# Optimization experiments

Hardware: AMD Instinct MI355X
Metric: run time of the kernel (lower is better)

The kernel has to match this reference:

```python
import jax, jax.numpy as jnp
import numpy as np
from jax import lax

PALETTE = 256


def setup_inputs() -> dict:
    key = jax.random.key(0)
    k1, k2, k3, k4 = jax.random.split(key, 4)
    x = jax.random.normal(k1, (16, 64, 256, 256), dtype=jnp.float32)
    lookup_table = jax.random.normal(k2, (PALETTE,), dtype=jnp.float32) * 0.05
    weight_idx = jax.random.randint(k3, (64, 64, 3, 3), 0, PALETTE, dtype=jnp.int32)
    bias = jax.random.normal(k4, (64,), dtype=jnp.float32) * 0.01
    return {"x": x, "lookup_table": lookup_table, "weight_idx": weight_idx, "bias": bias}


def reference(x, lookup_table, weight_idx, bias):
    # Dequantize: palette gather produces full OIHW weight tensor.
    full_w = lookup_table[weight_idx]  # [O, I, kH, kW] float32
    # conv2d with stride=1, padding=0 (hardcoded in module), dilation=1, groups=1
    out = lax.conv_general_dilated(
        x, full_w,
        window_strides=(1, 1),
        padding='VALID',
        rhs_dilation=(1, 1),
        dimension_numbers=('NCHW', 'OIHW', 'NCHW'),
        feature_group_count=1,
    )
    return out + bias[None, :, None, None]
```

## Files before the change

kernel.cpp:

```cpp
#include <hip/hip_runtime.h>


typedef __bf16 bf16x8 __attribute__((ext_vector_type(8)));
typedef float f32x4 __attribute__((ext_vector_type(4)));

union Frag {
    uint4 q;
    bf16x8 v;
};

__global__ __launch_bounds__(256) void dequant_B(
        const float* __restrict__ lut, const int* __restrict__ widx,
        uint4* __restrict__ Bws) {
    int s = blockIdx.x * 256 + threadIdx.x;
    int l = s & 63;
    int nt = (s >> 6) & 3;
    int kc = s >> 8;
    if (kc >= 18) return;
    int r = kc >> 1;
    int kh = r / 3, kw = r - kh * 3;
    int o = nt * 16 + (l & 15);
    int c0 = (kc & 1) * 32 + (l >> 4) * 8;
    Frag f;
#pragma unroll
    for (int j = 0; j < 8; ++j) {
        int c = c0 + j;
        int idx = widx[((o * 64 + c) * 3 + kh) * 3 + kw];
        f.v[j] = (__bf16)lut[idx];
    }
    Bws[s] = f.q;
}

#define LDS_PIX 396

__global__ __launch_bounds__(256, 3) void conv_mfma(
        const float* __restrict__ x, const float* __restrict__ bias,
        const uint4* __restrict__ Bws, float* __restrict__ out) {
    __shared__ uint4 ldsA[8 * LDS_PIX];
    unsigned* lds32 = (unsigned*)ldsA;

    int bx = blockIdx.x;
    int ow0 = (bx & 3) * 64;
    int oh0 = ((bx >> 2) & 63) * 4;
    int n = bx >> 8;
    int t = threadIdx.x;

    const float* xn = x + (size_t)n * (64 * 256 * 256);

    int w = t >> 6;
    int l = t & 63;
    int l15 = l & 15, l4 = l >> 4;

    {
        int colg = l15;
        int chp  = l4;
        const float* xw = xn + ow0 + colg * 4;
#pragma unroll
        for (int cc = 0; cc < 2; ++cc) {
            int cb = w + cc * 4;
            const float* cbase = xw + (cb * 8 + chp * 2) * 65536;
            f32x4 f0[6], f1[6];
#pragma unroll
            for (int rr = 0; rr < 6; ++rr) {
                int y = oh0 + rr; if (y > 255) y = 255;
                const float* p = cbase + y * 256;
                f0[rr] = *(const f32x4*)(p);
                f1[rr] = *(const f32x4*)(p + 65536);
            }
#pragma unroll
            for (int rr = 0; rr < 6; ++rr) {
                int gbase = cb * LDS_PIX + rr * 66 + colg * 4;
#pragma unroll
                for (int i = 0; i < 4; ++i) {
                    union { __bf16 h[2]; unsigned u; } bp;
                    bp.h[0] = (__bf16)f0[rr][i];
                    bp.h[1] = (__bf16)f1[rr][i];
                    lds32[(gbase + i) * 4 + chp] = bp.u;
                }
            }
        }
        if (t < 96) {
            int cblk = t & 7;
            int rc = t >> 3;
            int rr = rc >> 1;
            int col2 = 64 + (rc & 1);
            int y = oh0 + rr; if (y > 255) y = 255;
            int xc = ow0 + col2; if (xc > 255) xc = 255;
            const float* src = xn + cblk * 8 * 65536 + y * 256 + xc;
            Frag f;
#pragma unroll
            for (int j = 0; j < 8; ++j)
                f.v[j] = (__bf16)src[j * 65536];
            ldsA[cblk * LDS_PIX + rr * 66 + col2] = f.q;
        }
    }
    __syncthreads();

    f32x4 acc[4][4] = {};

    for (int kc = 0; kc < 18; ++kc) {
        int r = kc >> 1;
        int kh = r / 3, kw = r - kh * 3;
        int cblk = (kc & 1) * 4 + l4;
        int pix = (w + kh) * 66 + l15 + kw;

        Frag b[4];
#pragma unroll
        for (int nt = 0; nt < 4; ++nt)
            b[nt].q = Bws[(kc * 4 + nt) * 64 + l];

        Frag a[4];
#pragma unroll
        for (int mt = 0; mt < 4; ++mt)
            a[mt].q = ldsA[cblk * LDS_PIX + pix + mt * 16];

#pragma unroll
        for (int mt = 0; mt < 4; ++mt)
#pragma unroll
            for (int nt = 0; nt < 4; ++nt)
                acc[mt][nt] = __builtin_amdgcn_mfma_f32_16x16x32_bf16(
                    a[mt].v, b[nt].v, acc[mt][nt], 0, 0, 0);
    }

    __syncthreads();
    float* slab = (float*)ldsA + w * (16 * 65);

    int oh = oh0 + w;
    if (oh < 254) {
        float* orow = out + (((size_t)n * 64) * 254 + oh) * 254 + ow0;
        bool colok = (ow0 + l) < 254;
#pragma unroll
        for (int nt = 0; nt < 4; ++nt) {
#pragma unroll
            for (int mt = 0; mt < 4; ++mt)
#pragma unroll
                for (int rg = 0; rg < 4; ++rg)
                    slab[l15 * 65 + mt * 16 + l4 * 4 + rg] = acc[mt][nt][rg];
#pragma unroll
            for (int j = 0; j < 16; ++j) {
                int o = nt * 16 + j;
                float v = slab[j * 65 + l] + bias[o];
                if (colok)
                    orow[(size_t)o * (254 * 254) + l] = v;
            }
        }
    }
}

extern "C" void kernel_launch(void* const* d_in, const int* in_sizes, int n_in,
                              void* d_out, int out_size, void* d_ws, size_t ws_size,
                              hipStream_t stream) {
    const float* x    = (const float*)d_in[0];
    const float* lut  = (const float*)d_in[1];
    const int*   widx = (const int*)d_in[2];
    const float* bias = (const float*)d_in[3];
    float* out = (float*)d_out;
    uint4* Bws = (uint4*)d_ws;

    dequant_B<<<18, 256, 0, stream>>>(lut, widx, Bws);
    conv_mfma<<<4096, 256, 0, stream>>>(x, bias, (const uint4*)Bws, out);
}
```

Measured before the change: 511.9 us.

## Split conv input channels into two halves and stage weights in LDS

The conv kernel now handles the 64 input channels in two halves of 32. Each half loads its activation tile and its slice of dequantized weights into shared memory, then runs 9 MFMA steps that read both operands from LDS instead of global memory. This shrinks the A tile per phase and swaps per-iteration global loads of B fragments for LDS reads. In exchange it adds an extra barrier phase, uses a larger combined LDS buffer, and lowers the occupancy hint from 3 to 2 blocks per CU.

```diff
diff --git a/kernel.cpp b/kernel.cpp
--- a/kernel.cpp
+++ b/kernel.cpp
@@ -31,13 +31,15 @@
     Bws[s] = f.q;
 }
 
-#define LDS_PIX 396
+#define A_PIX 396
 
-__global__ __launch_bounds__(256, 3) void conv_mfma(
+__global__ __launch_bounds__(256, 2) void conv_mfma(
         const float* __restrict__ x, const float* __restrict__ bias,
         const uint4* __restrict__ Bws, float* __restrict__ out) {
-    __shared__ uint4 ldsA[8 * LDS_PIX];
-    unsigned* lds32 = (unsigned*)ldsA;
+    __shared__ uint4 lds[3888];
+    uint4* ldsA = lds;
+    uint4* ldsB = lds + 1584;
+    unsigned* lds32 = (unsigned*)lds;
 
     int bx = blockIdx.x;
     int ow0 = (bx & 3) * 64;
@@ -51,14 +53,24 @@
     int l = t & 63;
     int l15 = l & 15, l4 = l >> 4;
 
-    {
-        int colg = l15;
-        int chp  = l4;
-        const float* xw = xn + ow0 + colg * 4;
+    int tl_cb  = t & 3;
+    int tl_rc  = t >> 2;
+    int tl_rr  = tl_rc >> 1;
+    int tl_col = 64 + (tl_rc & 1);
+    int tl_xc  = ow0 + tl_col; if (tl_xc > 255) tl_xc = 255;
+
+    f32x4 acc[4][4] = {};
+
+    for (int h = 0; h < 2; ++h) {
+        uint4 breg[9];
 #pragma unroll
-        for (int cc = 0; cc < 2; ++cc) {
-            int cb = w + cc * 4;
-            const float* cbase = xw + (cb * 8 + chp * 2) * 65536;
+        for (int i = 0; i < 9; ++i)
+            breg[i] = Bws[((2 * i + h) * 4 + w) * 64 + l];
+
+        {
+            int colg = l15, chp = l4;
+            const float* cbase = xn + ((h * 4 + w) * 8 + chp * 2) * 65536
+                                 + ow0 + colg * 4;
             f32x4 f0[6], f1[6];
 #pragma unroll
             for (int rr = 0; rr < 6; ++rr) {
@@ -69,61 +81,59 @@
             }
 #pragma unroll
             for (int rr = 0; rr < 6; ++rr) {
-                int gbase = cb * LDS_PIX + rr * 66 + colg * 4;
+                int gbase = w * A_PIX + rr * 66 + colg * 4;
 #pragma unroll
                 for (int i = 0; i < 4; ++i) {
-                    union { __bf16 h[2]; unsigned u; } bp;
-                    bp.h[0] = (__bf16)f0[rr][i];
-                    bp.h[1] = (__bf16)f1[rr][i];
+                    union { __bf16 hh[2]; unsigned u; } bp;
+                    bp.hh[0] = (__bf16)f0[rr][i];
+                    bp.hh[1] = (__bf16)f1[rr][i];
                     lds32[(gbase + i) * 4 + chp] = bp.u;
                 }
             }
+            if (t < 48) {
+                int y = oh0 + tl_rr; if (y > 255) y = 255;
+                const float* src = xn + ((h * 4 + tl_cb) * 8) * 65536
+                                   + y * 256 + tl_xc;
+                Frag f;
+#pragma unroll
+                for (int j = 0; j < 8; ++j)
+                    f.v[j] = (__bf16)src[j * 65536];
+                ldsA[tl_cb * A_PIX + tl_rr * 66 + tl_col] = f.q;
+            }
         }
-        if (t < 96) {
-            int cblk = t & 7;
-            int rc = t >> 3;
-            int rr = rc >> 1;
-            int col2 = 64 + (rc & 1);
-            int y = oh0 + rr; if (y > 255) y = 255;
-            int xc = ow0 + col2; if (xc > 255) xc = 255;
-            const float* src = xn + cblk * 8 * 65536 + y * 256 + xc;
-            Frag f;
-#pragma unroll
-            for (int j = 0; j < 8; ++j)
-                f.v[j] = (__bf16)src[j * 65536];
-            ldsA[cblk * LDS_PIX + rr * 66 + col2] = f.q;
-        }
-    }
-    __syncthreads();
-
-    f32x4 acc[4][4] = {};
-
-    for (int kc = 0; kc < 18; ++kc) {
-        int r = kc >> 1;
-        int kh = r / 3, kw = r - kh * 3;
-        int cblk = (kc & 1) * 4 + l4;
-        int pix = (w + kh) * 66 + l15 + kw;
-
-        Frag b[4];
-#pragma unroll
-        for (int nt = 0; nt < 4; ++nt)
-            b[nt].q = Bws[(kc * 4 + nt) * 64 + l];
-
-        Frag a[4];
-#pragma unroll
-        for (int mt = 0; mt < 4; ++mt)
-            a[mt].q = ldsA[cblk * LDS_PIX + pix + mt * 16];
 
 #pragma unroll
-        for (int mt = 0; mt < 4; ++mt)
+        for (int i = 0; i < 9; ++i)
+            ldsB[(i * 4 + w) * 64 + l] = breg[i];
+
+        __syncthreads();
+
+#pragma unroll
+        for (int i = 0; i < 9; ++i) {
+            int kh = i / 3, kw = i - kh * 3;
+            int pix = (w + kh) * 66 + l15 + kw;
+
+            Frag b[4];
 #pragma unroll
             for (int nt = 0; nt < 4; ++nt)
-                acc[mt][nt] = __builtin_amdgcn_mfma_f32_16x16x32_bf16(
-                    a[mt].v, b[nt].v, acc[mt][nt], 0, 0, 0);
+                b[nt].q = ldsB[(i * 4 + nt) * 64 + l];
+
+            Frag a[4];
+#pragma unroll
+            for (int mt = 0; mt < 4; ++mt)
+                a[mt].q = ldsA[l4 * A_PIX + pix + mt * 16];
+
+#pragma unroll
+            for (int mt = 0; mt < 4; ++mt)
+#pragma unroll
+                for (int nt = 0; nt < 4; ++nt)
+                    acc[mt][nt] = __builtin_amdgcn_mfma_f32_16x16x32_bf16(
+                        a[mt].v, b[nt].v, acc[mt][nt], 0, 0, 0);
+        }
+        __syncthreads();
     }
 
-    __syncthreads();
-    float* slab = (float*)ldsA + w * (16 * 65);
+    float* slab = (float*)lds + w * (16 * 65);
 
     int oh = oh0 + w;
     if (oh < 254) {
```

After: 555.8 us. +8.6%, slower.
